# Kernel optimization log

Hardware: AMD Instinct MI355X
Metric: run time of the kernel (lower is better)

## Reference

```python
import jax, jax.numpy as jnp
import numpy as np

B, H, W = 16, 512, 512
NF, EMB, HEADS, NCLS, G = 1024, 768, 12, 4, 16

# segment start indices: RL pts 0:44, LL 44:94, heart 94:120 (groups not connected)
_SEG_STARTS = np.concatenate([np.arange(0, 43), np.arange(44, 93), np.arange(94, 119)])
# num_regions==6 ROI boxes mapped to the 16x16 grid: rows int(b0*16):int(b2*16), cols int(b1*16):int(b3*16)
_BOXES = [(0, 6, 0, 8), (4, 11, 0, 8), (9, 16, 0, 8), (0, 6, 8, 16), (4, 11, 8, 16), (9, 16, 8, 16)]


def _rasterize(landmarks):
    # vectorized replacement of the per-point index_put_/arange loops
    pts = jnp.clip((landmarks * H).astype(jnp.int32), 0, H - 1)   # [B,120,2] (x,y)
    p1 = pts[:, _SEG_STARTS]                                      # [B,S,2]
    p2 = pts[:, _SEG_STARTS + 1]
    k = jnp.arange(H)                                             # max steps per segment
    dy = p2[..., 1] - p1[..., 1]
    dx = p2[..., 0] - p1[..., 0]
    valid = (k < dy[..., None]) & (k < dx[..., None])             # [B,S,K]
    yi = jnp.clip(p1[..., 1:2] + k, 0, H - 1)
    xi = jnp.clip(p1[..., 0:1] + k, 0, W - 1)
    b = jnp.arange(landmarks.shape[0])[:, None, None]
    flat = ((b * H + yi) * W + xi).reshape(-1)
    mask = jnp.zeros(landmarks.shape[0] * H * W, jnp.float32)
    mask = mask.at[flat].max(valid.reshape(-1).astype(jnp.float32))
    return mask.reshape(-1, 1, H, W)


def _affine_grid(theta):
    # torch.nn.functional.affine_grid, align_corners=False
    xs = (2.0 * jnp.arange(W) + 1.0) / W - 1.0
    ys = (2.0 * jnp.arange(H) + 1.0) / H - 1.0
    gx, gy = jnp.meshgrid(xs, ys)                                 # [H,W]
    base = jnp.stack([gx, gy, jnp.ones_like(gx)], -1)             # [H,W,3]
    return jnp.einsum('hwk,bjk->bhwj', base, theta)               # [B,H,W,2]


def _grid_sample(img, grid):
    # bilinear, zero padding, align_corners=False
    Bs, C, Hi, Wi = img.shape
    fx = ((grid[..., 0] + 1.0) * Wi - 1.0) * 0.5
    fy = ((grid[..., 1] + 1.0) * Hi - 1.0) * 0.5
    x0, y0 = jnp.floor(fx), jnp.floor(fy)
    wx1, wy1 = fx - x0, fy - y0
    b = jnp.arange(Bs)[:, None, None]

    def gather(yi, xi):
        ok = (yi >= 0) & (yi < Hi) & (xi >= 0) & (xi < Wi)
        v = img[b, :, jnp.clip(yi, 0, Hi - 1).astype(jnp.int32), jnp.clip(xi, 0, Wi - 1).astype(jnp.int32)]  # [B,H,W,C]
        return v * ok[..., None]

    out = (gather(y0, x0) * ((1 - wy1) * (1 - wx1))[..., None]
           + gather(y0, x0 + 1) * ((1 - wy1) * wx1)[..., None]
           + gather(y0 + 1, x0) * (wy1 * (1 - wx1))[..., None]
           + gather(y0 + 1, x0 + 1) * (wy1 * wx1)[..., None])
    return out.transpose(0, 3, 1, 2)


def _ln(x, g, b):
    m = x.mean(-1, keepdims=True)
    v = ((x - m) ** 2).mean(-1, keepdims=True)
    return (x - m) / jnp.sqrt(v + 1e-5) * g + b


def _pool_rois(x):
    outs = [jax.image.resize(x[:, :, r0:r1, c0:c1], (x.shape[0], x.shape[1], G, G), 'bilinear')
            for r0, r1, c0, c1 in _BOXES]
    return jnp.stack(outs, 1)                                     # [B,6,C,16,16]


def _forward(x, landmarks, stn_w1, stn_b1, stn_w2, stn_b2, conv_w, conv_b, pe_w, pe_b, pos,
             ln1_g, ln1_b, qkv_w, qkv_b, proj_w, proj_b, ln2_g, ln2_b,
             mlp_w1, mlp_b1, mlp_w2, mlp_b2, fc_w, fc_b):
    seg_mask = jax.lax.stop_gradient(_rasterize(landmarks))       # frozen no_grad seg path
    # STN localization: pool mask -> dense(50) -> dense(6) affine theta
    pooled = seg_mask.reshape(B, 1, 32, H // 32, 32, W // 32).mean((3, 5))
    h = jnp.tanh(pooled.reshape(B, -1) @ stn_w1 + stn_b1)
    theta = (h @ stn_w2 + stn_b2).reshape(B, 2, 3)
    grid = _affine_grid(theta)
    transformed_mask = _grid_sample(seg_mask, grid)
    transformed_img = _grid_sample(x, grid)
    # backbone stand-in: stride-32 conv 512->16, num_features=1024
    feat = jax.lax.conv_general_dilated(transformed_img, conv_w, (32, 32), 'VALID')
    feat = jax.nn.relu(feat + conv_b[None, :, None, None])        # [B,NF,16,16]
    tok = feat.reshape(B, NF, G * G).transpose(0, 2, 1) @ pe_w + pe_b + pos
    # one pre-norm transformer encoder block
    t = _ln(tok, ln1_g, ln1_b)
    qkv = (t @ qkv_w + qkv_b).reshape(B, G * G, 3, HEADS, EMB // HEADS)
    q, k, v = qkv[:, :, 0], qkv[:, :, 1], qkv[:, :, 2]
    attn = jax.nn.softmax(jnp.einsum('bqhd,bkhd->bhqk', q, k) / np.sqrt(EMB // HEADS).astype(np.float32), -1)
    o = jnp.einsum('bhqk,bkhd->bqhd', attn, v).reshape(B, G * G, EMB)
    tok = tok + o @ proj_w + proj_b
    t2 = _ln(tok, ln2_g, ln2_b)
    tok = tok + jax.nn.gelu(t2 @ mlp_w1 + mlp_b1) @ mlp_w2 + mlp_b2
    fmap = tok.reshape(B, G, G, EMB).transpose(0, 3, 1, 2)        # [B,768,16,16]
    feats = _pool_rois(fmap).mean((-2, -1))                       # [B,6,768] ROI-GAP
    scores = jax.nn.softmax(feats @ fc_w + fc_b, -1)              # [B,6,4]
    return scores, transformed_img, transformed_mask


def setup_inputs():
    key = jax.random.key(0)
    ks = jax.random.split(key, 12)
    s = 0.02
    return dict(
        x=jax.random.normal(ks[0], (B, 3, H, W), jnp.float32),
        landmarks=jax.random.uniform(ks[1], (B, 120, 2), jnp.float32),
        stn_w1=jax.random.normal(ks[2], (1024, 50), jnp.float32) * s,
        stn_b1=jnp.zeros(50, jnp.float32),
        stn_w2=jax.random.normal(ks[3], (50, 6), jnp.float32) * 0.001,
        stn_b2=jnp.array([1.0, 0.0, 0.0, 0.0, 1.0, 0.0], jnp.float32),
        conv_w=jax.random.normal(ks[4], (NF, 3, 32, 32), jnp.float32) * s,
        conv_b=jnp.zeros(NF, jnp.float32),
        pe_w=jax.random.normal(ks[5], (NF, EMB), jnp.float32) * s,
        pe_b=jnp.zeros(EMB, jnp.float32),
        pos=jax.random.normal(ks[6], (G * G, EMB), jnp.float32) * s,
        ln1_g=jnp.ones(EMB, jnp.float32), ln1_b=jnp.zeros(EMB, jnp.float32),
        qkv_w=jax.random.normal(ks[7], (EMB, 3 * EMB), jnp.float32) * s,
        qkv_b=jnp.zeros(3 * EMB, jnp.float32),
        proj_w=jax.random.normal(ks[8], (EMB, EMB), jnp.float32) * s,
        proj_b=jnp.zeros(EMB, jnp.float32),
        ln2_g=jnp.ones(EMB, jnp.float32), ln2_b=jnp.zeros(EMB, jnp.float32),
        mlp_w1=jax.random.normal(ks[9], (EMB, 4 * EMB), jnp.float32) * s,
        mlp_b1=jnp.zeros(4 * EMB, jnp.float32),
        mlp_w2=jax.random.normal(ks[10], (4 * EMB, EMB), jnp.float32) * s,
        mlp_b2=jnp.zeros(EMB, jnp.float32),
        fc_w=jax.random.normal(ks[11], (EMB, NCLS), jnp.float32) * s,
        fc_b=jnp.zeros(NCLS, jnp.float32),
    )


def reference(x, landmarks, stn_w1, stn_b1, stn_w2, stn_b2, conv_w, conv_b, pe_w, pe_b, pos,
              ln1_g, ln1_b, qkv_w, qkv_b, proj_w, proj_b, ln2_g, ln2_b,
              mlp_w1, mlp_b1, mlp_w2, mlp_b2, fc_w, fc_b):
    return _forward(x, landmarks, stn_w1, stn_b1, stn_w2, stn_b2, conv_w, conv_b, pe_w, pe_b, pos,
                    ln1_g, ln1_b, qkv_w, qkv_b, proj_w, proj_b, ln2_g, ln2_b,
                    mlp_w1, mlp_b1, mlp_w2, mlp_b2, fc_w, fc_b)
```

## Files before the change

kernel.cpp:

```cpp
#include <hip/hip_runtime.h>
#include <hip/hip_bf16.h>
#include <cstdint>


#define B_    16
#define HH    512
#define WW    512
#define NF_   1024
#define EMB_  768
#define HEADS_ 12
#define NTOK  256
#define M_    (B_*NTOK)
#define KCONV 3072

typedef __bf16 bf16_t;
typedef __bf16 bf16x8 __attribute__((ext_vector_type(8)));
typedef float  f32x4  __attribute__((ext_vector_type(4)));

typedef __attribute__((address_space(1))) const void* gas_t;
typedef __attribute__((address_space(3))) void* las_t;

__device__ __forceinline__ void gload16(const bf16_t* g, bf16_t* l) {
    __builtin_amdgcn_global_load_lds((gas_t)g, (las_t)l, 16, 0, 0);
}

__device__ __forceinline__ float tanh_fast(float x) {
    return 1.0f - 2.0f / (__expf(2.0f * x) + 1.0f);
}

__global__ __launch_bounds__(128)
void raster_kernel(const float* __restrict__ lm, float* __restrict__ seg) {
    int b = blockIdx.x;
    int s = threadIdx.x;
    if (s >= 117) return;
    int seg0 = (s < 43) ? s : ((s < 92) ? s + 1 : s + 2);
    const float* p = lm + (size_t)b * 240;
    int p1x = min(max((int)(p[seg0*2 + 0] * 512.0f), 0), 511);
    int p1y = min(max((int)(p[seg0*2 + 1] * 512.0f), 0), 511);
    int p2x = min(max((int)(p[(seg0+1)*2 + 0] * 512.0f), 0), 511);
    int p2y = min(max((int)(p[(seg0+1)*2 + 1] * 512.0f), 0), 511);
    int dy = p2y - p1y, dx = p2x - p1x;
    int kmax = min(dy, dx);
    float* sb = seg + (size_t)b * (HH*WW);
    for (int k = 0; k < kmax; ++k) {
        int yi = min(p1y + k, 511);
        int xi = min(p1x + k, 511);
        sb[yi*WW + xi] = 1.0f;
    }
}

__global__ __launch_bounds__(256)
void pool_kernel(const float* __restrict__ seg, float* __restrict__ pooled) {
    int idx = blockIdx.x * 256 + threadIdx.x;
    int ox = idx & 31, oy = (idx >> 5) & 31, b = idx >> 10;
    const float* sb = seg + (size_t)b * (HH*WW) + (oy*16)*WW + ox*16;
    float s = 0.0f;
    for (int dy = 0; dy < 16; ++dy) {
        #pragma unroll
        for (int dx = 0; dx < 16; ++dx) s += sb[dy*WW + dx];
    }
    pooled[idx] = s * (1.0f/256.0f);
}

__global__ __launch_bounds__(256)
void transpose_w1_kernel(const float* __restrict__ in, float* __restrict__ out) {
    int idx = blockIdx.x * 256 + threadIdx.x;
    int j = idx >> 10, k = idx & 1023;
    out[idx] = in[k*50 + j];
}

__global__ __launch_bounds__(1024)
void stn2_kernel(const float* __restrict__ pooled, const float* __restrict__ w1t,
                 const float* __restrict__ b1, const float* __restrict__ w2,
                 const float* __restrict__ b2, float* __restrict__ theta) {
    __shared__ float pl[1024];
    __shared__ float hl[56];
    int b = blockIdx.x, tid = threadIdx.x;
    pl[tid] = pooled[b*1024 + tid];
    __syncthreads();
    int wave = tid >> 6, lane = tid & 63;
    #pragma unroll
    for (int p = 0; p < 4; ++p) {
        int j = wave + (p << 4);
        if (j < 50) {
            const float* wr = w1t + j*1024;
            float acc = 0.0f;
            #pragma unroll
            for (int i = 0; i < 16; ++i) {
                int k = lane + (i << 6);
                acc = fmaf(pl[k], wr[k], acc);
            }
            #pragma unroll
            for (int off = 32; off; off >>= 1) acc += __shfl_xor(acc, off);
            if (lane == 0) hl[j] = tanhf(acc + b1[j]);
        }
    }
    __syncthreads();
    if (tid < 6) {
        float acc = b2[tid];
        for (int k = 0; k < 50; ++k) acc = fmaf(hl[k], w2[k*6 + tid], acc);
        theta[b*6 + tid] = acc;
    }
}

__global__ __launch_bounds__(256)
void gridsample_kernel(const float* __restrict__ x, const float* __restrict__ seg,
                       const float* __restrict__ theta,
                       float* __restrict__ timg, float* __restrict__ tmask,
                       bf16_t* __restrict__ timgb) {
    size_t idx = (size_t)blockIdx.x * 256 + threadIdx.x;
    int xx = (int)(idx & 511);
    int yy = (int)((idx >> 9) & 511);
    int b  = (int)(idx >> 18);
    __shared__ float th[6];
    if (threadIdx.x < 6) th[threadIdx.x] = theta[b*6 + threadIdx.x];
    __syncthreads();
    float gx = (2.0f*xx + 1.0f) * (1.0f/512.0f) - 1.0f;
    float gy = (2.0f*yy + 1.0f) * (1.0f/512.0f) - 1.0f;
    float g0 = gx*th[0] + gy*th[1] + th[2];
    float g1 = gx*th[3] + gy*th[4] + th[5];
    float fx = ((g0 + 1.0f)*512.0f - 1.0f)*0.5f;
    float fy = ((g1 + 1.0f)*512.0f - 1.0f)*0.5f;
    float x0f = floorf(fx), y0f = floorf(fy);
    float wx1 = fx - x0f,  wy1 = fy - y0f;
    int ix0 = (int)x0f, iy0 = (int)y0f;
    int ix1 = ix0 + 1,  iy1 = iy0 + 1;
    float fy0ok = (iy0 >= 0 && iy0 < HH) ? 1.0f : 0.0f;
    float fy1ok = (iy1 >= 0 && iy1 < HH) ? 1.0f : 0.0f;
    float fx0ok = (ix0 >= 0 && ix0 < WW) ? 1.0f : 0.0f;
    float fx1ok = (ix1 >= 0 && ix1 < WW) ? 1.0f : 0.0f;
    float w00 = (1.0f-wy1)*(1.0f-wx1) * fy0ok * fx0ok;
    float w01 = (1.0f-wy1)*wx1        * fy0ok * fx1ok;
    float w10 = wy1*(1.0f-wx1)        * fy1ok * fx0ok;
    float w11 = wy1*wx1               * fy1ok * fx1ok;
    int cx0 = min(max(ix0,0),511), cx1 = min(max(ix1,0),511);
    int cy0 = min(max(iy0,0),511), cy1 = min(max(iy1,0),511);
    int i00 = cy0*WW + cx0, i01 = cy0*WW + cx1, i10 = cy1*WW + cx0, i11 = cy1*WW + cx1;
    size_t pix = (size_t)yy*WW + xx;
    #pragma unroll
    for (int c = 0; c < 3; ++c) {
        const float* pl = x + ((size_t)(b*3 + c)) * (HH*WW);
        float v = w00*pl[i00] + w01*pl[i01] + w10*pl[i10] + w11*pl[i11];
        timg [((size_t)(b*3 + c))*(HH*WW) + pix] = v;
        timgb[((size_t)(b*3 + c))*(HH*WW) + pix] = (bf16_t)v;
    }
    const float* sp = seg + (size_t)b * (HH*WW);
    float mv = w00*sp[i00] + w01*sp[i01] + w10*sp[i10] + w11*sp[i11];
    tmask[(size_t)b*(HH*WW) + pix] = mv;
}

__global__ __launch_bounds__(256)
void convert_bf16_kernel(const float* __restrict__ in, bf16_t* __restrict__ out) {
    int idx = (blockIdx.x * 256 + threadIdx.x) * 8;
    float4 v0 = *reinterpret_cast<const float4*>(in + idx);
    float4 v1 = *reinterpret_cast<const float4*>(in + idx + 4);
    bf16x8 o;
    o[0]=(bf16_t)v0.x; o[1]=(bf16_t)v0.y; o[2]=(bf16_t)v0.z; o[3]=(bf16_t)v0.w;
    o[4]=(bf16_t)v1.x; o[5]=(bf16_t)v1.y; o[6]=(bf16_t)v1.z; o[7]=(bf16_t)v1.w;
    *reinterpret_cast<bf16x8*>(out + idx) = o;
}

__global__ __launch_bounds__(256)
void transpose_bf16_kernel(const float* __restrict__ in, bf16_t* __restrict__ out,
                           int K, int N) {
    __shared__ float tile[32][33];
    int bk = blockIdx.y * 32, bn = blockIdx.x * 32;
    int r = threadIdx.x >> 5, c = threadIdx.x & 31;
    #pragma unroll
    for (int i = 0; i < 4; ++i)
        tile[r + 8*i][c] = in[(size_t)(bk + r + 8*i) * N + bn + c];
    __syncthreads();
    #pragma unroll
    for (int i = 0; i < 4; ++i)
        out[(size_t)(bn + r + 8*i) * K + bk + c] = (bf16_t)tile[c][r + 8*i];
}

enum { EPI_CONV=0, EPI_PE=1, EPI_QKV=2, EPI_PROJ=3, EPI_GELU=4, EPI_MLP2=5 };

template<int EPI>
__device__ __forceinline__ void gemm_epilogue64(
        f32x4 (&acc)[2][2], const float* bias, const float* extra,
        float* Cf, bf16_t* Cb, int bm, int bn, int wm, int wn,
        int rr, int g, int N) {
    #pragma unroll
    for (int i = 0; i < 2; ++i) {
        #pragma unroll
        for (int j = 0; j < 2; ++j) {
            #pragma unroll
            for (int r = 0; r < 4; ++r) {
                int m = bm + wm + i*16 + g*4 + r;
                int n = bn + wn + j*16 + rr;
                size_t o = (size_t)m * N + n;
                float v = acc[i][j][r] + bias[n];
                if (EPI == EPI_CONV) {
                    Cb[o] = (bf16_t)fmaxf(v, 0.0f);
                } else if (EPI == EPI_PE) {
                    Cf[o] = v + extra[(size_t)(m & 255)*N + n];
                } else if (EPI == EPI_QKV) {
                    Cb[o] = (bf16_t)v;
                } else if (EPI == EPI_PROJ || EPI == EPI_MLP2) {
                    Cf[o] = v + Cf[o];
                } else if (EPI == EPI_GELU) {
                    float u = v;
                    float gl = 0.5f*u*(1.0f + tanh_fast(0.7978845608028654f*(u + 0.044715f*u*u*u)));
                    Cb[o] = (bf16_t)gl;
                }
            }
        }
    }
}

template<int EPI>
__global__ __launch_bounds__(256)
void gemm64_kernel(const bf16_t* __restrict__ A, const bf16_t* __restrict__ Bt,
                   const float* __restrict__ bias, const float* __restrict__ extra,
                   float* __restrict__ Cf, bf16_t* __restrict__ Cb,
                   int M, int N, int K) {
    __shared__ __align__(16) bf16_t As[2][64*64];
    __shared__ __align__(16) bf16_t Bs[2][64*64];
    const int tid = threadIdx.x;
    const int nN   = N >> 6;
    const int nblk = (M >> 6) * nN;
    const int q    = nblk >> 3;
    const int id   = (blockIdx.x & 7) * q + (blockIdx.x >> 3);
    const int bm = (id / nN) * 64, bn = (id % nN) * 64;
    const int lane = tid & 63, w = tid >> 6;
    const int rr = lane & 15, g = lane >> 4;
    const int wm = (w & 1) * 32, wn = (w >> 1) * 32;
    const int sr = tid >> 3;
    const int sc = ((tid & 7) ^ (sr & 7)) * 8;
    const bf16_t* gA0 = A  + (size_t)(bm + sr)      * K + sc;
    const bf16_t* gA1 = A  + (size_t)(bm + 32 + sr) * K + sc;
    const bf16_t* gB0 = Bt + (size_t)(bn + sr)      * K + sc;
    const bf16_t* gB1 = Bt + (size_t)(bn + 32 + sr) * K + sc;

    auto STAGE = [&](int buf, int k0) {
        gload16(gA0 + k0, As[buf] + w*512);
        gload16(gA1 + k0, As[buf] + 2048 + w*512);
        gload16(gB0 + k0, Bs[buf] + w*512);
        gload16(gB1 + k0, Bs[buf] + 2048 + w*512);
    };

    const int s0 = (0*4 + g) ^ (rr & 7);
    const int s1 = (1*4 + g) ^ (rr & 7);

    f32x4 acc[2][2] = {};
    STAGE(0, 0);
    __syncthreads();
    int cur = 0;
    for (int k0 = 0; k0 < K; k0 += 64) {
        if (k0 + 64 < K) STAGE(cur ^ 1, k0 + 64);
        bf16x8 af[2][2], bfv[2][2];
        #pragma unroll
        for (int i = 0; i < 2; ++i) {
            int ra = (wm + i*16 + rr) * 64;
            af[i][0] = *reinterpret_cast<const bf16x8*>(As[cur] + ra + s0*8);
            af[i][1] = *reinterpret_cast<const bf16x8*>(As[cur] + ra + s1*8);
            int rb = (wn + i*16 + rr) * 64;
            bfv[i][0] = *reinterpret_cast<const bf16x8*>(Bs[cur] + rb + s0*8);
            bfv[i][1] = *reinterpret_cast<const bf16x8*>(Bs[cur] + rb + s1*8);
        }
        #pragma unroll
        for (int ks = 0; ks < 2; ++ks)
            #pragma unroll
            for (int i = 0; i < 2; ++i)
                #pragma unroll
                for (int j = 0; j < 2; ++j)
                    acc[i][j] = __builtin_amdgcn_mfma_f32_16x16x32_bf16(
                        af[i][ks], bfv[j][ks], acc[i][j], 0, 0, 0);
        __syncthreads();
        cur ^= 1;
    }
    gemm_epilogue64<EPI>(acc, bias, extra, Cf, Cb, bm, bn, wm, wn, rr, g, N);
}

__global__ __launch_bounds__(256)
void gemm_conv64_kernel(const bf16_t* __restrict__ timgb, const bf16_t* __restrict__ Bt,
                        const float* __restrict__ bias, bf16_t* __restrict__ Cb) {
    const int N = NF_, K = KCONV;
    __shared__ __align__(16) bf16_t As[2][64*64];
    __shared__ __align__(16) bf16_t Bs[2][64*64];
    const int tid = threadIdx.x;
    const int nN   = N >> 6;
    const int nblk = (M_ >> 6) * nN;
    const int q    = nblk >> 3;
    const int id   = (blockIdx.x & 7) * q + (blockIdx.x >> 3);
    const int bm = (id / nN) * 64, bn = (id % nN) * 64;
    const int lane = tid & 63, w = tid >> 6;
    const int rr = lane & 15, g = lane >> 4;
    const int wm = (w & 1) * 32, wn = (w >> 1) * 32;
    const int sr = tid >> 3;
    const int s  = (tid & 7) ^ (sr & 7);
    int row0 = bm + sr, row1 = bm + 32 + sr;
    int b0 = row0 >> 8, py0 = (row0 >> 4) & 15, px0 = row0 & 15;
    int b1 = row1 >> 8, py1 = (row1 >> 4) & 15, px1 = row1 & 15;
    size_t off0 = (size_t)b0*786432 + py0*16384 + px0*32 + (s>>2)*512 + (s&3)*8;
    size_t off1 = (size_t)b1*786432 + py1*16384 + px1*32 + (s>>2)*512 + (s&3)*8;
    const bf16_t* gB0 = Bt + (size_t)(bn + sr)      * K + s*8;
    const bf16_t* gB1 = Bt + (size_t)(bn + 32 + sr) * K + s*8;

    auto STAGE = [&](int buf, int k0) {
        int c   = k0 >> 10;
        int ky0 = (k0 >> 5) & 31;
        size_t koff = (size_t)c*262144 + (size_t)ky0*512;
        gload16(timgb + off0 + koff, As[buf] + w*512);
        gload16(timgb + off1 + koff, As[buf] + 2048 + w*512);
        gload16(gB0 + k0, Bs[buf] + w*512);
        gload16(gB1 + k0, Bs[buf] + 2048 + w*512);
    };

    const int s0 = (0*4 + g) ^ (rr & 7);
    const int s1 = (1*4 + g) ^ (rr & 7);

    f32x4 acc[2][2] = {};
    STAGE(0, 0);
    __syncthreads();
    int cur = 0;
    for (int k0 = 0; k0 < K; k0 += 64) {
        if (k0 + 64 < K) STAGE(cur ^ 1, k0 + 64);
        bf16x8 af[2][2], bfv[2][2];
        #pragma unroll
        for (int i = 0; i < 2; ++i) {
            int ra = (wm + i*16 + rr) * 64;
            af[i][0] = *reinterpret_cast<const bf16x8*>(As[cur] + ra + s0*8);
            af[i][1] = *reinterpret_cast<const bf16x8*>(As[cur] + ra + s1*8);
            int rb = (wn + i*16 + rr) * 64;
            bfv[i][0] = *reinterpret_cast<const bf16x8*>(Bs[cur] + rb + s0*8);
            bfv[i][1] = *reinterpret_cast<const bf16x8*>(Bs[cur] + rb + s1*8);
        }
        #pragma unroll
        for (int ks = 0; ks < 2; ++ks)
            #pragma unroll
            for (int i = 0; i < 2; ++i)
                #pragma unroll
                for (int j = 0; j < 2; ++j)
                    acc[i][j] = __builtin_amdgcn_mfma_f32_16x16x32_bf16(
                        af[i][ks], bfv[j][ks], acc[i][j], 0, 0, 0);
        __syncthreads();
        cur ^= 1;
    }
    gemm_epilogue64<EPI_CONV>(acc, bias, nullptr, nullptr, Cb, bm, bn, wm, wn, rr, g, N);
}

__global__ __launch_bounds__(256)
void ln_kernel(const float* __restrict__ x, const float* __restrict__ g,
               const float* __restrict__ be, bf16_t* __restrict__ out) {
    int r = blockIdx.x, tid = threadIdx.x;
    const float* xr = x + (size_t)r * EMB_;
    float v0 = xr[tid], v1 = xr[tid+256], v2 = xr[tid+512];
    float s = v0+v1+v2, s2 = v0*v0 + v1*v1 + v2*v2;
    __shared__ float red[8];
    #pragma unroll
    for (int off = 32; off; off >>= 1) { s += __shfl_xor(s, off); s2 += __shfl_xor(s2, off); }
    if ((tid & 63) == 0) { red[tid>>6] = s; red[4 + (tid>>6)] = s2; }
    __syncthreads();
    s  = red[0]+red[1]+red[2]+red[3];
    s2 = red[4]+red[5]+red[6]+red[7];
    float mean = s * (1.0f/768.0f);
    float var  = s2 * (1.0f/768.0f) - mean*mean;
    float rstd = rsqrtf(var + 1e-5f);
    bf16_t* orow = out + (size_t)r * EMB_;
    orow[tid]     = (bf16_t)((v0-mean)*rstd*g[tid]     + be[tid]);
    orow[tid+256] = (bf16_t)((v1-mean)*rstd*g[tid+256] + be[tid+256]);
    orow[tid+512] = (bf16_t)((v2-mean)*rstd*g[tid+512] + be[tid+512]);
}

__global__ __launch_bounds__(256)
void attn_kernel5(const bf16_t* __restrict__ qkv, bf16_t* __restrict__ o) {
    __shared__ __align__(16) bf16_t Ks[256*72];
    __shared__ __align__(16) bf16_t Vt[64*264];
    __shared__ __align__(16) bf16_t Ps[4][64*72];
    const int tid  = threadIdx.x;
    const int lane = tid & 63, w = tid >> 6;
    const int rr   = lane & 15, g = lane >> 4;
    const int h = blockIdx.x % HEADS_;
    const int b = blockIdx.x / HEADS_;
    const bf16_t* base = qkv + (size_t)(b*256)*2304;

    {
        const bf16_t* kr = base + (size_t)tid*2304 + 768  + h*64;
        const bf16_t* vr = base + (size_t)tid*2304 + 1536 + h*64;
        bf16_t* kd = Ks + tid*72;
        #pragma unroll
        for (int c2 = 0; c2 < 8; ++c2) {
            *reinterpret_cast<bf16x8*>(kd + c2*8) =
                *reinterpret_cast<const bf16x8*>(kr + c2*8);
            bf16x8 v = *reinterpret_cast<const bf16x8*>(vr + c2*8);
            #pragma unroll
            for (int e = 0; e < 8; ++e)
                Vt[(c2*8 + e)*264 + tid] = v[e];
        }
    }

    bf16x8 qf[4][2];
    #pragma unroll
    for (int i = 0; i < 4; ++i)
        #pragma unroll
        for (int ks = 0; ks < 2; ++ks)
            qf[i][ks] = *reinterpret_cast<const bf16x8*>(
                base + (size_t)(w*64 + i*16 + rr)*2304 + h*64 + ks*32 + g*8);

    f32x4 oacc[4][4] = {};
    float lacc[4][4] = {};
    __syncthreads();

    bf16_t* Pw = Ps[w];
    for (int kc = 0; kc < 4; ++kc) {
        f32x4 sacc[4][4] = {};
        #pragma unroll
        for (int ks = 0; ks < 2; ++ks) {
            bf16x8 kf[4];
            #pragma unroll
            for (int j = 0; j < 4; ++j)
                kf[j] = *reinterpret_cast<const bf16x8*>(
                    Ks + (size_t)(kc*64 + j*16 + rr)*72 + ks*32 + g*8);
            #pragma unroll
            for (int i = 0; i < 4; ++i)
                #pragma unroll
                for (int j = 0; j < 4; ++j)
                    sacc[i][j] = __builtin_amdgcn_mfma_f32_16x16x32_bf16(
                        qf[i][ks], kf[j], sacc[i][j], 0, 0, 0);
        }
        #pragma unroll
        for (int i = 0; i < 4; ++i) {
            #pragma unroll
            for (int r = 0; r < 4; ++r) {
                int prow = i*16 + g*4 + r;
                float ps = 0.0f;
                #pragma unroll
                for (int j = 0; j < 4; ++j) {
                    float p = __expf(sacc[i][j][r] * 0.125f);
                    ps += p;
                    Pw[prow*72 + j*16 + rr] = (bf16_t)p;
                }
                lacc[i][r] += ps;
            }
        }
        #pragma unroll
        for (int ks = 0; ks < 2; ++ks) {
            bf16x8 pa[4], vb[4];
            #pragma unroll
            for (int i = 0; i < 4; ++i)
                pa[i] = *reinterpret_cast<const bf16x8*>(
                    Pw + (size_t)(i*16 + rr)*72 + ks*32 + g*8);
            #pragma unroll
            for (int n = 0; n < 4; ++n)
                vb[n] = *reinterpret_cast<const bf16x8*>(
                    Vt + (size_t)(n*16 + rr)*264 + kc*64 + ks*32 + g*8);
            #pragma unroll
            for (int i = 0; i < 4; ++i)
                #pragma unroll
                for (int n = 0; n < 4; ++n)
                    oacc[i][n] = __builtin_amdgcn_mfma_f32_16x16x32_bf16(
                        pa[i], vb[n], oacc[i][n], 0, 0, 0);
        }
    }

    #pragma unroll
    for (int i = 0; i < 4; ++i) {
        #pragma unroll
        for (int r = 0; r < 4; ++r) {
            float v = lacc[i][r];
            v += __shfl_xor(v, 1);
            v += __shfl_xor(v, 2);
            v += __shfl_xor(v, 4);
            v += __shfl_xor(v, 8);
            lacc[i][r] = 1.0f / v;
        }
    }
    #pragma unroll
    for (int i = 0; i < 4; ++i) {
        #pragma unroll
        for (int r = 0; r < 4; ++r) {
            int qrow = w*64 + i*16 + g*4 + r;
            bf16_t* orow = o + (size_t)(b*256 + qrow)*EMB_ + h*64;
            float inv = lacc[i][r];
            #pragma unroll
            for (int n = 0; n < 4; ++n)
                orow[n*16 + rr] = (bf16_t)(oacc[i][n][r] * inv);
        }
    }
}

__global__ __launch_bounds__(256)
void head_kernel(const float* __restrict__ tok, const float* __restrict__ fcw,
                 const float* __restrict__ fcb, float* __restrict__ scores) {
    const int bx[6][4] = {{0,6,0,8},{4,11,0,8},{9,16,0,8},{0,6,8,16},{4,11,8,16},{9,16,8,16}};
    int box = blockIdx.x % 6, b = blockIdx.x / 6;
    int r0 = bx[box][0], r1 = bx[box][1], c0 = bx[box][2], c1 = bx[box][3];
    int rh = r1 - r0, rw = c1 - c0;
    __shared__ float wl[256];
    __shared__ float feats[768];
    __shared__ float red[4];
    int tid = threadIdx.x;
    int py = tid >> 4, px = tid & 15;
    float w = 0.0f;
    if (py >= r0 && py < r1 && px >= c0 && px < c1) {
        int ly = py - r0, lx = px - c0;
        float cy = 0.0f, cx = 0.0f;
        for (int o = 0; o < 16; ++o) {
            float sy = (o + 0.5f) * (float)rh * (1.0f/16.0f) - 0.5f;
            sy = fminf(fmaxf(sy, 0.0f), (float)(rh - 1));
            int i0 = (int)floorf(sy); float t = sy - (float)i0;
            if (ly == i0)     cy += 1.0f - t;
            if (ly == i0 + 1) cy += t;
            float sx = (o + 0.5f) * (float)rw * (1.0f/16.0f) - 0.5f;
            sx = fminf(fmaxf(sx, 0.0f), (float)(rw - 1));
            int j0 = (int)floorf(sx); float u = sx - (float)j0;
            if (lx == j0)     cx += 1.0f - u;
            if (lx == j0 + 1) cx += u;
        }
        w = (cy * (1.0f/16.0f)) * (cx * (1.0f/16.0f));
    }
    wl[tid] = w;
    __syncthreads();
    for (int e = tid; e < EMB_; e += 256) {
        float f = 0.0f;
        for (int iy = r0; iy < r1; ++iy)
            for (int ix = c0; ix < c1; ++ix) {
                int p = iy*16 + ix;
                f += wl[p] * tok[((size_t)(b*256 + p))*EMB_ + e];
            }
        feats[e] = f;
    }
    __syncthreads();
    float lg[4];
    #pragma unroll
    for (int cc = 0; cc < 4; ++cc) {
        float part = 0.0f;
        for (int e = tid; e < EMB_; e += 256) part += feats[e]*fcw[e*4 + cc];
        #pragma unroll
        for (int off = 32; off; off >>= 1) part += __shfl_xor(part, off);
        __syncthreads();
        if ((tid & 63) == 0) red[tid>>6] = part;
        __syncthreads();
        lg[cc] = red[0]+red[1]+red[2]+red[3] + fcb[cc];
    }
    if (tid == 0) {
        float mx = fmaxf(fmaxf(lg[0],lg[1]), fmaxf(lg[2],lg[3]));
        float e0 = expf(lg[0]-mx), e1 = expf(lg[1]-mx), e2 = expf(lg[2]-mx), e3 = expf(lg[3]-mx);
        float inv = 1.0f/(e0+e1+e2+e3);
        float* out = scores + (size_t)(b*6 + box)*4;
        out[0] = e0*inv; out[1] = e1*inv; out[2] = e2*inv; out[3] = e3*inv;
    }
}

extern "C" void kernel_launch(void* const* d_in, const int* in_sizes, int n_in,
                              void* d_out, int out_size, void* d_ws, size_t ws_size,
                              hipStream_t stream) {
    (void)in_sizes; (void)n_in; (void)out_size; (void)ws_size;
    const float* x       = (const float*)d_in[0];
    const float* lm      = (const float*)d_in[1];
    const float* stn_w1  = (const float*)d_in[2];
    const float* stn_b1  = (const float*)d_in[3];
    const float* stn_w2  = (const float*)d_in[4];
    const float* stn_b2  = (const float*)d_in[5];
    const float* conv_w  = (const float*)d_in[6];
    const float* conv_b  = (const float*)d_in[7];
    const float* pe_w    = (const float*)d_in[8];
    const float* pe_b    = (const float*)d_in[9];
    const float* pos     = (const float*)d_in[10];
    const float* ln1_g   = (const float*)d_in[11];
    const float* ln1_b   = (const float*)d_in[12];
    const float* qkv_w   = (const float*)d_in[13];
    const float* qkv_b   = (const float*)d_in[14];
    const float* proj_w  = (const float*)d_in[15];
    const float* proj_b  = (const float*)d_in[16];
    const float* ln2_g   = (const float*)d_in[17];
    const float* ln2_b   = (const float*)d_in[18];
    const float* mlp_w1  = (const float*)d_in[19];
    const float* mlp_b1  = (const float*)d_in[20];
    const float* mlp_w2  = (const float*)d_in[21];
    const float* mlp_b2  = (const float*)d_in[22];
    const float* fc_w    = (const float*)d_in[23];
    const float* fc_b    = (const float*)d_in[24];

    float* out    = (float*)d_out;
    float* scores = out;
    float* timg   = out + 384;
    float* tmask  = out + 384 + (size_t)B_*3*HH*WW;

    char* ws = (char*)d_ws;
    size_t off = 0;
    auto alloc = [&](size_t bytes) {
        off = (off + 255) & ~(size_t)255;
        void* p = ws + off; off += bytes; return p;
    };
    char*   slotBig = (char*)alloc(25165824);
    char*   slotT   = (char*)alloc((size_t)B_*3*HH*WW*2);
    char*   slotC   = (char*)alloc((size_t)M_*NF_*2);
    float*  tok     = (float*)alloc((size_t)M_*EMB_*4);
    bf16_t* tbuf    = (bf16_t*)alloc((size_t)M_*EMB_*2);
    bf16_t* conv_wb = (bf16_t*)alloc((size_t)NF_*KCONV*2);
    bf16_t* pe_wb   = (bf16_t*)alloc((size_t)EMB_*NF_*2);
    bf16_t* qkv_wb  = (bf16_t*)alloc((size_t)3*EMB_*EMB_*2);
    bf16_t* proj_wb = (bf16_t*)alloc((size_t)EMB_*EMB_*2);
    bf16_t* mlp1_wb = (bf16_t*)alloc((size_t)4*EMB_*EMB_*2);
    bf16_t* mlp2_wb = (bf16_t*)alloc((size_t)EMB_*4*EMB_*2);
    float*  w1t     = (float*)alloc(50*1024*4);
    float*  pooled  = (float*)alloc(16384*4);
    float*  theta   = (float*)alloc(96*4);

    float*  seg    = (float*)slotBig;
    bf16_t* hidden = (bf16_t*)slotBig;
    bf16_t* timgb  = (bf16_t*)slotT;
    bf16_t* qkvb   = (bf16_t*)slotT;
    bf16_t* featC  = (bf16_t*)slotC;
    bf16_t* obuf   = (bf16_t*)slotC;

    convert_bf16_kernel<<<(NF_*KCONV)/8/256, 256, 0, stream>>>(conv_w, conv_wb);
    transpose_bf16_kernel<<<dim3(EMB_/32, NF_/32),    256, 0, stream>>>(pe_w,   pe_wb,   NF_,  EMB_);
    transpose_bf16_kernel<<<dim3(3*EMB_/32, EMB_/32), 256, 0, stream>>>(qkv_w,  qkv_wb,  EMB_, 3*EMB_);
    transpose_bf16_kernel<<<dim3(EMB_/32, EMB_/32),   256, 0, stream>>>(proj_w, proj_wb, EMB_, EMB_);
    transpose_bf16_kernel<<<dim3(4*EMB_/32, EMB_/32), 256, 0, stream>>>(mlp_w1, mlp1_wb, EMB_, 4*EMB_);
    transpose_bf16_kernel<<<dim3(EMB_/32, 4*EMB_/32), 256, 0, stream>>>(mlp_w2, mlp2_wb, 4*EMB_, EMB_);
    transpose_w1_kernel<<<200, 256, 0, stream>>>(stn_w1, w1t);

    hipMemsetAsync(seg, 0, (size_t)B_*HH*WW*sizeof(float), stream);
    raster_kernel<<<B_, 128, 0, stream>>>(lm, seg);
    pool_kernel<<<64, 256, 0, stream>>>(seg, pooled);
    stn2_kernel<<<B_, 1024, 0, stream>>>(pooled, w1t, stn_b1, stn_w2, stn_b2, theta);
    gridsample_kernel<<<(B_*HH*WW)/256, 256, 0, stream>>>(x, seg, theta, timg, tmask, timgb);

    gemm_conv64_kernel<<<(M_/64)*(NF_/64), 256, 0, stream>>>(
        timgb, conv_wb, conv_b, featC);

    gemm64_kernel<EPI_PE><<<(M_/64)*(EMB_/64), 256, 0, stream>>>(
        featC, pe_wb, pe_b, pos, tok, nullptr, M_, EMB_, NF_);

    ln_kernel<<<M_, 256, 0, stream>>>(tok, ln1_g, ln1_b, tbuf);
    gemm64_kernel<EPI_QKV><<<(M_/64)*(3*EMB_/64), 256, 0, stream>>>(
        tbuf, qkv_wb, qkv_b, nullptr, nullptr, qkvb, M_, 3*EMB_, EMB_);

    attn_kernel5<<<B_*HEADS_, 256, 0, stream>>>(qkvb, obuf);

    gemm64_kernel<EPI_PROJ><<<(M_/64)*(EMB_/64), 256, 0, stream>>>(
        obuf, proj_wb, proj_b, nullptr, tok, nullptr, M_, EMB_, EMB_);

    ln_kernel<<<M_, 256, 0, stream>>>(tok, ln2_g, ln2_b, tbuf);
    gemm64_kernel<EPI_GELU><<<(M_/64)*(4*EMB_/64), 256, 0, stream>>>(
        tbuf, mlp1_wb, mlp_b1, nullptr, nullptr, hidden, M_, 4*EMB_, EMB_);
    gemm64_kernel<EPI_MLP2><<<(M_/64)*(EMB_/64), 256, 0, stream>>>(
        hidden, mlp2_wb, mlp_b2, nullptr, tok, nullptr, M_, EMB_, 4*EMB_);

    head_kernel<<<B_*6, 256, 0, stream>>>(tok, fc_w, fc_b, scores);
}
```

Measured before the change: 339.6 us.

## Merge weight-prep kernels, fuse pooling into STN, store residual stream in bf16

Folds the conv-weight conversion, STN weight transpose and all GEMM weight transposes into one launch. It also folds average pooling into the STN MLP kernel and widens the head kernel to 768 threads, one per embedding channel. The residual token stream changes from fp32 to bf16, which halves its read and write traffic in the PE, proj, MLP2, layernorm and head stages. Keeping the residual in bf16 risks accuracy drift across the residual adds, and the single-block-per-image pooling in the STN kernel gives less parallelism than the separate pool kernel had.

```diff
diff --git a/kernel.cpp b/kernel.cpp
--- a/kernel.cpp
+++ b/kernel.cpp
@@ -50,33 +50,68 @@
 }
 
 __global__ __launch_bounds__(256)
-void pool_kernel(const float* __restrict__ seg, float* __restrict__ pooled) {
-    int idx = blockIdx.x * 256 + threadIdx.x;
-    int ox = idx & 31, oy = (idx >> 5) & 31, b = idx >> 10;
-    const float* sb = seg + (size_t)b * (HH*WW) + (oy*16)*WW + ox*16;
-    float s = 0.0f;
-    for (int dy = 0; dy < 16; ++dy) {
-        #pragma unroll
-        for (int dx = 0; dx < 16; ++dx) s += sb[dy*WW + dx];
-    }
-    pooled[idx] = s * (1.0f/256.0f);
-}
-
-__global__ __launch_bounds__(256)
-void transpose_w1_kernel(const float* __restrict__ in, float* __restrict__ out) {
-    int idx = blockIdx.x * 256 + threadIdx.x;
-    int j = idx >> 10, k = idx & 1023;
-    out[idx] = in[k*50 + j];
+void prep_weights_kernel(const float* __restrict__ conv_w, bf16_t* __restrict__ conv_wb,
+                         const float* __restrict__ stn_w1, float* __restrict__ w1t,
+                         const float* __restrict__ pe_w,   bf16_t* __restrict__ pe_wb,
+                         const float* __restrict__ qkv_w,  bf16_t* __restrict__ qkv_wb,
+                         const float* __restrict__ proj_w, bf16_t* __restrict__ proj_wb,
+                         const float* __restrict__ mlp_w1, bf16_t* __restrict__ mlp1_wb,
+                         const float* __restrict__ mlp_w2, bf16_t* __restrict__ mlp2_wb) {
+    __shared__ float tile[32][33];
+    int id = blockIdx.x, tid = threadIdx.x;
+    if (id < 1536) {
+        int idx = (id*256 + tid) * 8;
+        float4 v0 = *reinterpret_cast<const float4*>(conv_w + idx);
+        float4 v1 = *reinterpret_cast<const float4*>(conv_w + idx + 4);
+        bf16x8 o;
+        o[0]=(bf16_t)v0.x; o[1]=(bf16_t)v0.y; o[2]=(bf16_t)v0.z; o[3]=(bf16_t)v0.w;
+        o[4]=(bf16_t)v1.x; o[5]=(bf16_t)v1.y; o[6]=(bf16_t)v1.z; o[7]=(bf16_t)v1.w;
+        *reinterpret_cast<bf16x8*>(conv_wb + idx) = o;
+        return;
+    }
+    id -= 1536;
+    if (id < 200) {
+        int idx = id*256 + tid;
+        int j = idx >> 10, k = idx & 1023;
+        w1t[idx] = stn_w1[k*50 + j];
+        return;
+    }
+    id -= 200;
+    const float* in; bf16_t* out; int K, N;
+    if      (id < 768)  { in = pe_w;   out = pe_wb;   K = 1024; N = 768;  }
+    else if (id < 2496) { in = qkv_w;  out = qkv_wb;  K = 768;  N = 2304; id -= 768;  }
+    else if (id < 3072) { in = proj_w; out = proj_wb; K = 768;  N = 768;  id -= 2496; }
+    else if (id < 5376) { in = mlp_w1; out = mlp1_wb; K = 768;  N = 3072; id -= 3072; }
+    else                { in = mlp_w2; out = mlp2_wb; K = 3072; N = 768;  id -= 5376; }
+    int nb = N >> 5;
+    int bn = (id % nb) * 32, bk = (id / nb) * 32;
+    int r = tid >> 5, c = tid & 31;
+    #pragma unroll
+    for (int i = 0; i < 4; ++i)
+        tile[r + 8*i][c] = in[(size_t)(bk + r + 8*i) * N + bn + c];
+    __syncthreads();
+    #pragma unroll
+    for (int i = 0; i < 4; ++i)
+        out[(size_t)(bn + r + 8*i) * K + bk + c] = (bf16_t)tile[c][r + 8*i];
 }
 
 __global__ __launch_bounds__(1024)
-void stn2_kernel(const float* __restrict__ pooled, const float* __restrict__ w1t,
+void stn3_kernel(const float* __restrict__ seg, const float* __restrict__ w1t,
                  const float* __restrict__ b1, const float* __restrict__ w2,
                  const float* __restrict__ b2, float* __restrict__ theta) {
     __shared__ float pl[1024];
     __shared__ float hl[56];
     int b = blockIdx.x, tid = threadIdx.x;
-    pl[tid] = pooled[b*1024 + tid];
+    {
+        int ox = tid & 31, oy = tid >> 5;
+        const float* sb = seg + (size_t)b*(HH*WW) + (oy*16)*WW + ox*16;
+        float s = 0.0f;
+        for (int dy = 0; dy < 16; ++dy) {
+            #pragma unroll
+            for (int dx = 0; dx < 16; ++dx) s += sb[dy*WW + dx];
+        }
+        pl[tid] = s * (1.0f/256.0f);
+    }
     __syncthreads();
     int wave = tid >> 6, lane = tid & 63;
     #pragma unroll
@@ -149,38 +184,12 @@
     tmask[(size_t)b*(HH*WW) + pix] = mv;
 }
 
-__global__ __launch_bounds__(256)
-void convert_bf16_kernel(const float* __restrict__ in, bf16_t* __restrict__ out) {
-    int idx = (blockIdx.x * 256 + threadIdx.x) * 8;
-    float4 v0 = *reinterpret_cast<const float4*>(in + idx);
-    float4 v1 = *reinterpret_cast<const float4*>(in + idx + 4);
-    bf16x8 o;
-    o[0]=(bf16_t)v0.x; o[1]=(bf16_t)v0.y; o[2]=(bf16_t)v0.z; o[3]=(bf16_t)v0.w;
-    o[4]=(bf16_t)v1.x; o[5]=(bf16_t)v1.y; o[6]=(bf16_t)v1.z; o[7]=(bf16_t)v1.w;
-    *reinterpret_cast<bf16x8*>(out + idx) = o;
-}
-
-__global__ __launch_bounds__(256)
-void transpose_bf16_kernel(const float* __restrict__ in, bf16_t* __restrict__ out,
-                           int K, int N) {
-    __shared__ float tile[32][33];
-    int bk = blockIdx.y * 32, bn = blockIdx.x * 32;
-    int r = threadIdx.x >> 5, c = threadIdx.x & 31;
-    #pragma unroll
-    for (int i = 0; i < 4; ++i)
-        tile[r + 8*i][c] = in[(size_t)(bk + r + 8*i) * N + bn + c];
-    __syncthreads();
-    #pragma unroll
-    for (int i = 0; i < 4; ++i)
-        out[(size_t)(bn + r + 8*i) * K + bk + c] = (bf16_t)tile[c][r + 8*i];
-}
-
 enum { EPI_CONV=0, EPI_PE=1, EPI_QKV=2, EPI_PROJ=3, EPI_GELU=4, EPI_MLP2=5 };
 
 template<int EPI>
 __device__ __forceinline__ void gemm_epilogue64(
         f32x4 (&acc)[2][2], const float* bias, const float* extra,
-        float* Cf, bf16_t* Cb, int bm, int bn, int wm, int wn,
+        bf16_t* Cb, int bm, int bn, int wm, int wn,
         int rr, int g, int N) {
     #pragma unroll
     for (int i = 0; i < 2; ++i) {
@@ -195,11 +204,11 @@
                 if (EPI == EPI_CONV) {
                     Cb[o] = (bf16_t)fmaxf(v, 0.0f);
                 } else if (EPI == EPI_PE) {
-                    Cf[o] = v + extra[(size_t)(m & 255)*N + n];
+                    Cb[o] = (bf16_t)(v + extra[(size_t)(m & 255)*N + n]);
                 } else if (EPI == EPI_QKV) {
                     Cb[o] = (bf16_t)v;
                 } else if (EPI == EPI_PROJ || EPI == EPI_MLP2) {
-                    Cf[o] = v + Cf[o];
+                    Cb[o] = (bf16_t)(v + (float)Cb[o]);
                 } else if (EPI == EPI_GELU) {
                     float u = v;
                     float gl = 0.5f*u*(1.0f + tanh_fast(0.7978845608028654f*(u + 0.044715f*u*u*u)));
@@ -214,7 +223,7 @@
 __global__ __launch_bounds__(256)
 void gemm64_kernel(const bf16_t* __restrict__ A, const bf16_t* __restrict__ Bt,
                    const float* __restrict__ bias, const float* __restrict__ extra,
-                   float* __restrict__ Cf, bf16_t* __restrict__ Cb,
+                   bf16_t* __restrict__ Cb,
                    int M, int N, int K) {
     __shared__ __align__(16) bf16_t As[2][64*64];
     __shared__ __align__(16) bf16_t Bs[2][64*64];
@@ -271,7 +280,7 @@
         __syncthreads();
         cur ^= 1;
     }
-    gemm_epilogue64<EPI>(acc, bias, extra, Cf, Cb, bm, bn, wm, wn, rr, g, N);
+    gemm_epilogue64<EPI>(acc, bias, extra, Cb, bm, bn, wm, wn, rr, g, N);
 }
 
 __global__ __launch_bounds__(256)
@@ -339,15 +348,15 @@
         __syncthreads();
         cur ^= 1;
     }
-    gemm_epilogue64<EPI_CONV>(acc, bias, nullptr, nullptr, Cb, bm, bn, wm, wn, rr, g, N);
+    gemm_epilogue64<EPI_CONV>(acc, bias, nullptr, Cb, bm, bn, wm, wn, rr, g, N);
 }
 
 __global__ __launch_bounds__(256)
-void ln_kernel(const float* __restrict__ x, const float* __restrict__ g,
+void ln_kernel(const bf16_t* __restrict__ x, const float* __restrict__ g,
                const float* __restrict__ be, bf16_t* __restrict__ out) {
     int r = blockIdx.x, tid = threadIdx.x;
-    const float* xr = x + (size_t)r * EMB_;
-    float v0 = xr[tid], v1 = xr[tid+256], v2 = xr[tid+512];
+    const bf16_t* xr = x + (size_t)r * EMB_;
+    float v0 = (float)xr[tid], v1 = (float)xr[tid+256], v2 = (float)xr[tid+512];
     float s = v0+v1+v2, s2 = v0*v0 + v1*v1 + v2*v2;
     __shared__ float red[8];
     #pragma unroll
@@ -482,61 +491,67 @@
     }
 }
 
-__global__ __launch_bounds__(256)
-void head_kernel(const float* __restrict__ tok, const float* __restrict__ fcw,
-                 const float* __restrict__ fcb, float* __restrict__ scores) {
+__global__ __launch_bounds__(768)
+void head_kernel2(const bf16_t* __restrict__ tok, const float* __restrict__ fcw,
+                  const float* __restrict__ fcb, float* __restrict__ scores) {
     const int bx[6][4] = {{0,6,0,8},{4,11,0,8},{9,16,0,8},{0,6,8,16},{4,11,8,16},{9,16,8,16}};
     int box = blockIdx.x % 6, b = blockIdx.x / 6;
     int r0 = bx[box][0], r1 = bx[box][1], c0 = bx[box][2], c1 = bx[box][3];
     int rh = r1 - r0, rw = c1 - c0;
     __shared__ float wl[256];
-    __shared__ float feats[768];
-    __shared__ float red[4];
+    __shared__ float red[48];
     int tid = threadIdx.x;
-    int py = tid >> 4, px = tid & 15;
-    float w = 0.0f;
-    if (py >= r0 && py < r1 && px >= c0 && px < c1) {
-        int ly = py - r0, lx = px - c0;
-        float cy = 0.0f, cx = 0.0f;
-        for (int o = 0; o < 16; ++o) {
-            float sy = (o + 0.5f) * (float)rh * (1.0f/16.0f) - 0.5f;
-            sy = fminf(fmaxf(sy, 0.0f), (float)(rh - 1));
-            int i0 = (int)floorf(sy); float t = sy - (float)i0;
-            if (ly == i0)     cy += 1.0f - t;
-            if (ly == i0 + 1) cy += t;
-            float sx = (o + 0.5f) * (float)rw * (1.0f/16.0f) - 0.5f;
-            sx = fminf(fmaxf(sx, 0.0f), (float)(rw - 1));
-            int j0 = (int)floorf(sx); float u = sx - (float)j0;
-            if (lx == j0)     cx += 1.0f - u;
-            if (lx == j0 + 1) cx += u;
-        }
-        w = (cy * (1.0f/16.0f)) * (cx * (1.0f/16.0f));
-    }
-    wl[tid] = w;
-    __syncthreads();
-    for (int e = tid; e < EMB_; e += 256) {
-        float f = 0.0f;
-        for (int iy = r0; iy < r1; ++iy)
-            for (int ix = c0; ix < c1; ++ix) {
-                int p = iy*16 + ix;
-                f += wl[p] * tok[((size_t)(b*256 + p))*EMB_ + e];
+    if (tid < 256) {
+        int py = tid >> 4, px = tid & 15;
+        float w = 0.0f;
+        if (py >= r0 && py < r1 && px >= c0 && px < c1) {
+            int ly = py - r0, lx = px - c0;
+            float cy = 0.0f, cx = 0.0f;
+            for (int o = 0; o < 16; ++o) {
+                float sy = (o + 0.5f) * (float)rh * (1.0f/16.0f) - 0.5f;
+                sy = fminf(fmaxf(sy, 0.0f), (float)(rh - 1));
+                int i0 = (int)floorf(sy); float t = sy - (float)i0;
+                if (ly == i0)     cy += 1.0f - t;
+                if (ly == i0 + 1) cy += t;
+                float sx = (o + 0.5f) * (float)rw * (1.0f/16.0f) - 0.5f;
+                sx = fminf(fmaxf(sx, 0.0f), (float)(rw - 1));
+                int j0 = (int)floorf(sx); float u = sx - (float)j0;
+                if (lx == j0)     cx += 1.0f - u;
+                if (lx == j0 + 1) cx += u;
             }
-        feats[e] = f;
-    }
-    __syncthreads();
-    float lg[4];
-    #pragma unroll
-    for (int cc = 0; cc < 4; ++cc) {
-        float part = 0.0f;
-        for (int e = tid; e < EMB_; e += 256) part += feats[e]*fcw[e*4 + cc];
-        #pragma unroll
-        for (int off = 32; off; off >>= 1) part += __shfl_xor(part, off);
-        __syncthreads();
-        if ((tid & 63) == 0) red[tid>>6] = part;
-        __syncthreads();
-        lg[cc] = red[0]+red[1]+red[2]+red[3] + fcb[cc];
-    }
+            w = (cy * (1.0f/16.0f)) * (cx * (1.0f/16.0f));
+        }
+        wl[tid] = w;
+    }
+    __syncthreads();
+    float f = 0.0f;
+    for (int iy = r0; iy < r1; ++iy)
+        for (int ix = c0; ix < c1; ++ix) {
+            int p = iy*16 + ix;
+            f = fmaf(wl[p], (float)tok[((size_t)(b*256 + p))*EMB_ + tid], f);
+        }
+    float p0 = f * fcw[tid*4+0];
+    float p1 = f * fcw[tid*4+1];
+    float p2 = f * fcw[tid*4+2];
+    float p3 = f * fcw[tid*4+3];
+    #pragma unroll
+    for (int off = 32; off; off >>= 1) {
+        p0 += __shfl_xor(p0, off); p1 += __shfl_xor(p1, off);
+        p2 += __shfl_xor(p2, off); p3 += __shfl_xor(p3, off);
+    }
+    int wv = tid >> 6;
+    if ((tid & 63) == 0) {
+        red[wv*4+0] = p0; red[wv*4+1] = p1; red[wv*4+2] = p2; red[wv*4+3] = p3;
+    }
+    __syncthreads();
     if (tid == 0) {
+        float lg[4];
+        #pragma unroll
+        for (int cc = 0; cc < 4; ++cc) {
+            float s = fcb[cc];
+            for (int v = 0; v < 12; ++v) s += red[v*4+cc];
+            lg[cc] = s;
+        }
         float mx = fmaxf(fmaxf(lg[0],lg[1]), fmaxf(lg[2],lg[3]));
         float e0 = expf(lg[0]-mx), e1 = expf(lg[1]-mx), e2 = expf(lg[2]-mx), e3 = expf(lg[3]-mx);
         float inv = 1.0f/(e0+e1+e2+e3);
@@ -589,7 +604,7 @@
     char*   slotBig = (char*)alloc(25165824);
     char*   slotT   = (char*)alloc((size_t)B_*3*HH*WW*2);
     char*   slotC   = (char*)alloc((size_t)M_*NF_*2);
-    float*  tok     = (float*)alloc((size_t)M_*EMB_*4);
+    bf16_t* tok     = (bf16_t*)alloc((size_t)M_*EMB_*2);
     bf16_t* tbuf    = (bf16_t*)alloc((size_t)M_*EMB_*2);
     bf16_t* conv_wb = (bf16_t*)alloc((size_t)NF_*KCONV*2);
     bf16_t* pe_wb   = (bf16_t*)alloc((size_t)EMB_*NF_*2);
@@ -598,7 +613,6 @@
     bf16_t* mlp1_wb = (bf16_t*)alloc((size_t)4*EMB_*EMB_*2);
     bf16_t* mlp2_wb = (bf16_t*)alloc((size_t)EMB_*4*EMB_*2);
     float*  w1t     = (float*)alloc(50*1024*4);
-    float*  pooled  = (float*)alloc(16384*4);
     float*  theta   = (float*)alloc(96*4);
 
     float*  seg    = (float*)slotBig;
@@ -608,40 +622,35 @@
     bf16_t* featC  = (bf16_t*)slotC;
     bf16_t* obuf   = (bf16_t*)slotC;
 
-    convert_bf16_kernel<<<(NF_*KCONV)/8/256, 256, 0, stream>>>(conv_w, conv_wb);
-    transpose_bf16_kernel<<<dim3(EMB_/32, NF_/32),    256, 0, stream>>>(pe_w,   pe_wb,   NF_,  EMB_);
-    transpose_bf16_kernel<<<dim3(3*EMB_/32, EMB_/32), 256, 0, stream>>>(qkv_w,  qkv_wb,  EMB_, 3*EMB_);
-    transpose_bf16_kernel<<<dim3(EMB_/32, EMB_/32),   256, 0, stream>>>(proj_w, proj_wb, EMB_, EMB_);
-    transpose_bf16_kernel<<<dim3(4*EMB_/32, EMB_/32), 256, 0, stream>>>(mlp_w1, mlp1_wb, EMB_, 4*EMB_);
-    transpose_bf16_kernel<<<dim3(EMB_/32, 4*EMB_/32), 256, 0, stream>>>(mlp_w2, mlp2_wb, 4*EMB_, EMB_);
-    transpose_w1_kernel<<<200, 256, 0, stream>>>(stn_w1, w1t);
+    prep_weights_kernel<<<9416, 256, 0, stream>>>(
+        conv_w, conv_wb, stn_w1, w1t, pe_w, pe_wb, qkv_w, qkv_wb,
+        proj_w, proj_wb, mlp_w1, mlp1_wb, mlp_w2, mlp2_wb);
 
     hipMemsetAsync(seg, 0, (size_t)B_*HH*WW*sizeof(float), stream);
     raster_kernel<<<B_, 128, 0, stream>>>(lm, seg);
-    pool_kernel<<<64, 256, 0, stream>>>(seg, pooled);
-    stn2_kernel<<<B_, 1024, 0, stream>>>(pooled, w1t, stn_b1, stn_w2, stn_b2, theta);
+    stn3_kernel<<<B_, 1024, 0, stream>>>(seg, w1t, stn_b1, stn_w2, stn_b2, theta);
     gridsample_kernel<<<(B_*HH*WW)/256, 256, 0, stream>>>(x, seg, theta, timg, tmask, timgb);
 
     gemm_conv64_kernel<<<(M_/64)*(NF_/64), 256, 0, stream>>>(
         timgb, conv_wb, conv_b, featC);
 
     gemm64_kernel<EPI_PE><<<(M_/64)*(EMB_/64), 256, 0, stream>>>(
-        featC, pe_wb, pe_b, pos, tok, nullptr, M_, EMB_, NF_);
+        featC, pe_wb, pe_b, pos, tok, M_, EMB_, NF_);
 
     ln_kernel<<<M_, 256, 0, stream>>>(tok, ln1_g, ln1_b, tbuf);
     gemm64_kernel<EPI_QKV><<<(M_/64)*(3*EMB_/64), 256, 0, stream>>>(
-        tbuf, qkv_wb, qkv_b, nullptr, nullptr, qkvb, M_, 3*EMB_, EMB_);
+        tbuf, qkv_wb, qkv_b, nullptr, qkvb, M_, 3*EMB_, EMB_);
 
     attn_kernel5<<<B_*HEADS_, 256, 0, stream>>>(qkvb, obuf);
 
     gemm64_kernel<EPI_PROJ><<<(M_/64)*(EMB_/64), 256, 0, stream>>>(
-        obuf, proj_wb, proj_b, nullptr, tok, nullptr, M_, EMB_, EMB_);
+        obuf, proj_wb, proj_b, nullptr, tok, M_, EMB_, EMB_);
 
     ln_kernel<<<M_, 256, 0, stream>>>(tok, ln2_g, ln2_b, tbuf);
     gemm64_kernel<EPI_GELU><<<(M_/64)*(4*EMB_/64), 256, 0, stream>>>(
-        tbuf, mlp1_wb, mlp_b1, nullptr, nullptr, hidden, M_, 4*EMB_, EMB_);
+        tbuf, mlp1_wb, mlp_b1, nullptr, hidden, M_, 4*EMB_, EMB_);
     gemm64_kernel<EPI_MLP2><<<(M_/64)*(EMB_/64), 256, 0, stream>>>(
-        hidden, mlp2_wb, mlp_b2, nullptr, tok, nullptr, M_, EMB_, 4*EMB_);
-
-    head_kernel<<<B_*6, 256, 0, stream>>>(tok, fc_w, fc_b, scores);
-}
+        hidden, mlp2_wb, mlp_b2, nullptr, tok, M_, EMB_, 4*EMB_);
+
+    head_kernel2<<<B_*6, 768, 0, stream>>>(tok, fc_w, fc_b, scores);
+}
```

After: 300.0 us. 1.13x faster.
